# Performance work log

Measured on AMD Instinct MI355X. Metric: run time of the kernel, lower is better.

## Reference

```python
import jax, jax.numpy as jnp
import numpy as np

N_NODES = 100000
N_EDGES = 6400000
N_ELEMENTS = 95  # covalent radii table size
P = 6  # envelope polynomial order (init kwarg p)


def setup_inputs() -> dict:
    key = jax.random.key(0)
    k1, k2, k3, k4 = jax.random.split(key, 4)
    z = jax.random.randint(k1, (N_NODES,), 1, 95)  # atomic numbers 1..94
    edge_distance = jax.random.uniform(k2, (N_EDGES,), jnp.float32, 0.5, 5.0)
    edge_index = jax.random.randint(k3, (2, N_EDGES), 0, N_NODES)
    covalent_radii = jax.random.uniform(k4, (N_ELEMENTS,), jnp.float32, 0.5, 2.0)
    return {
        "z": z,
        "edge_distance": edge_distance,
        "edge_index": edge_index,
        "a_factor": jnp.float32(0.4546),
        "Z_power": jnp.float32(0.0842),
        "screen_coefs": jnp.full((4,), 0.1663, jnp.float32),
        "screen_exps": jnp.full((4,), 0.0354, jnp.float32),
        "covalent_radii": covalent_radii,
    }


def reference(z, edge_distance, edge_index, a_factor, Z_power, screen_coefs, screen_exps, covalent_radii):
    sender, receiver = edge_index[0], edge_index[1]
    Z_u = z[sender]
    Z_v = z[receiver]
    Z_uf = Z_u.astype(edge_distance.dtype)
    Z_vf = Z_v.astype(edge_distance.dtype)

    # screening length a = a_factor * 0.529 / (Zu^zp + Zv^zp)
    a = a_factor * 0.529 / (Z_uf ** Z_power + Z_vf ** Z_power)
    r_over_a = edge_distance / a  # [E]

    # phi(x) = sum_i c_i * exp(-d_i * x)
    phi = jnp.sum(screen_coefs * jnp.exp(-screen_exps * r_over_a[:, None]), axis=-1)  # [E]

    v_edges = 14.3996 * Z_uf * Z_vf / edge_distance * phi

    # smooth cutoff envelope
    r_max = covalent_radii[Z_u] + covalent_radii[Z_v]
    t = edge_distance / r_max
    p = float(P)
    envelope = (1.0
                - (p + 1.0) * (p + 2.0) / 2.0 * t ** P
                + p * (p + 2.0) * t ** (P + 1)
                - p * (p + 1.0) / 2.0 * t ** (P + 2))
    envelope = envelope * (t < 1.0).astype(edge_distance.dtype)

    v_edges = 0.5 * v_edges * envelope

    # scatter-add per receiver node
    V_ZBL = jax.ops.segment_sum(v_edges, receiver, num_segments=z.shape[0])
    return V_ZBL
```

## Files before the change

### kernel.cpp

```cpp
#include <hip/hip_runtime.h>

#define N_ELEM 95
#define MAX_NODES 100096
#define ZW_WORDS (MAX_NODES / 4)
#define RS2 20480
#define MAX_R2 5
#define EBLK 256

typedef float f32x4 __attribute__((ext_vector_type(4)));
typedef int   i32x4 __attribute__((ext_vector_type(4)));
typedef unsigned int u32;
typedef u32 u32x4 __attribute__((ext_vector_type(4)));
typedef unsigned short u16;

__device__ __forceinline__ u32 bf16_rtn(float f) {
    u32 u = __float_as_uint(f);
    return (u + 0x7FFFu + ((u >> 16) & 1u)) >> 16;
}
__device__ __forceinline__ u32 f15_rtn(float f) {
    u32 u = __float_as_uint(f);
    return (u + 0xFFFFu + ((u >> 17) & 1u)) >> 17;
}

__device__ __forceinline__ void build_ztab(
    u32* s_zw, const int* __restrict__ z, int n_words, int n_nodes, int tid, int nthr)
{
    for (int w = tid; w < n_words; w += nthr) {
        const int i = w << 2;
        u32 v;
        if (i + 4 <= n_nodes) {
            const i32x4 zz = ((const i32x4*)z)[w];
            v = ((u32)zz.x & 0xffu) | (((u32)zz.y & 0xffu) << 8)
              | (((u32)zz.z & 0xffu) << 16) | (((u32)zz.w & 0xffu) << 24);
        } else {
            v = 0u;
            for (int k = 0; k < 4 && i + k < n_nodes; ++k)
                v |= ((u32)z[i + k] & 0xffu) << (8 * k);
        }
        s_zw[w] = v;
    }
}

__global__ __launch_bounds__(1024) void k_edge_pack(
    const int*   __restrict__ z,
    const float* __restrict__ dist,
    const int*   __restrict__ sender,
    const int*   __restrict__ recv,
    const float* __restrict__ a_factor_p,
    const float* __restrict__ z_power_p,
    const float* __restrict__ coefs,
    const float* __restrict__ exps,
    const float* __restrict__ cradii,
    u32*         __restrict__ pk,
    int n_edges, int n_words, int n_nodes, int W)
{
    __shared__ u32    s_zw[ZW_WORDS];
    __shared__ float2 s_tab[N_ELEM];
    __shared__ float  s_coef[4], s_exp[4], s_inv;

    const int tid = threadIdx.x;
    build_ztab(s_zw, z, n_words, n_nodes, tid, 1024);
    if (tid < N_ELEM) {
        float zp = z_power_p[0];
        s_tab[tid] = make_float2(__powf((float)tid, zp), cradii[tid]);
    }
    if (tid < 4) { s_coef[tid] = coefs[tid]; s_exp[tid] = exps[tid]; }
    if (tid == 0) s_inv = 1.0f / (a_factor_p[0] * 0.529f);
    __syncthreads();

    const unsigned char* s_zb = (const unsigned char*)s_zw;
    const float inv_pref = s_inv;
    const float c0 = s_coef[0], c1 = s_coef[1], c2 = s_coef[2], c3 = s_coef[3];
    const float e0 = s_exp[0],  e1 = s_exp[1],  e2 = s_exp[2],  e3 = s_exp[3];

    const int n_grp = n_edges >> 3;
    const int g0 = blockIdx.x * W;
    const int g1 = min(n_grp, g0 + W);

    for (int g = g0 + tid; g < g1; g += 1024) {
        const f32x4 dA = __builtin_nontemporal_load((const f32x4*)dist + 2 * g);
        const f32x4 dB = __builtin_nontemporal_load((const f32x4*)dist + 2 * g + 1);
        const i32x4 sA = __builtin_nontemporal_load((const i32x4*)sender + 2 * g);
        const i32x4 sB = __builtin_nontemporal_load((const i32x4*)sender + 2 * g + 1);
        const i32x4 rA = __builtin_nontemporal_load((const i32x4*)recv + 2 * g);
        const i32x4 rB = __builtin_nontemporal_load((const i32x4*)recv + 2 * g + 1);

        float dd[8] = {dA.x, dA.y, dA.z, dA.w, dB.x, dB.y, dB.z, dB.w};
        int   ss[8] = {sA.x, sA.y, sA.z, sA.w, sB.x, sB.y, sB.z, sB.w};
        int   rr[8] = {rA.x, rA.y, rA.z, rA.w, rB.x, rB.y, rB.z, rB.w};

        int zu[8], zv[8];
        #pragma unroll
        for (int k = 0; k < 8; ++k) zu[k] = s_zb[ss[k]];
        #pragma unroll
        for (int k = 0; k < 8; ++k) zv[k] = s_zb[rr[k]];

        u32 ww[8];
        #pragma unroll
        for (int k = 0; k < 8; ++k) {
            const float d = dd[k];
            const float2 tu = s_tab[zu[k]];
            const float2 tv = s_tab[zv[k]];
            const float rmax = tu.y + tv.y;
            float o = 0.0f;
            if (d < rmax) {
                const float t   = __fdividef(d, rmax);
                const float roa = d * (tu.x + tv.x) * inv_pref;
                const float phi = c0 * __expf(-e0 * roa)
                                + c1 * __expf(-e1 * roa)
                                + c2 * __expf(-e2 * roa)
                                + c3 * __expf(-e3 * roa);
                const float v   = 7.1998f * (float)(zu[k] * zv[k]) * phi
                                * __fdividef(1.0f, d);
                const float t2  = t * t;
                const float t6  = t2 * t2 * t2;
                o = v * (1.0f - t6 * (28.0f - 48.0f * t + 21.0f * t2));
            }
            ww[k] = ((u32)rr[k] << 15) | f15_rtn(o);
        }
        ((u32x4*)pk)[2 * g]     = (u32x4){ww[0], ww[1], ww[2], ww[3]};
        ((u32x4*)pk)[2 * g + 1] = (u32x4){ww[4], ww[5], ww[6], ww[7]};
    }

    if (blockIdx.x == gridDim.x - 1) {
        for (int i = (n_grp << 3) + tid; i < n_edges; i += 1024) {
            const float d  = dist[i];
            const int   a  = s_zb[sender[i]];
            const u32   rv = (u32)recv[i];
            const int   b  = s_zb[rv];
            const float2 tu = s_tab[a];
            const float2 tv = s_tab[b];
            const float rmax = tu.y + tv.y;
            float o = 0.0f;
            if (d < rmax) {
                const float t   = __fdividef(d, rmax);
                const float roa = d * (tu.x + tv.x) * inv_pref;
                const float phi = c0 * __expf(-e0 * roa)
                                + c1 * __expf(-e1 * roa)
                                + c2 * __expf(-e2 * roa)
                                + c3 * __expf(-e3 * roa);
                const float v   = 7.1998f * (float)(a * b) * phi * __fdividef(1.0f, d);
                const float t2  = t * t;
                const float t6  = t2 * t2 * t2;
                o = v * (1.0f - t6 * (28.0f - 48.0f * t + 21.0f * t2));
            }
            pk[i] = (rv << 15) | f15_rtn(o);
        }
    }
}

__global__ __launch_bounds__(1024, 2) void k_accum4(
    const u32* __restrict__ pk,
    u16*       __restrict__ copies,
    int n_edges, int E8, int Q8, int C, int Rr)
{
    __shared__ float acc[RS2];
    const int c = blockIdx.x % C;
    const int r = blockIdx.x / C;
    const int tid = threadIdx.x;

    const u32 lo = (u32)r * RS2;
    const int q0 = c * Q8;
    const int q1 = min(E8, q0 + Q8);

    int q = q0 + tid;
    u32x4 wA = {0,0,0,0}, wB = {0,0,0,0};
    bool have = (q < q1);
    if (have) {
        wA = ((const u32x4*)pk)[2 * q];
        wB = ((const u32x4*)pk)[2 * q + 1];
    }

    for (int i = tid; i < RS2; i += 1024) acc[i] = 0.0f;
    __syncthreads();

    while (have) {
        const int qn = q + 1024;
        u32x4 nA = {0,0,0,0}, nB = {0,0,0,0};
        const bool hn = (qn < q1);
        if (hn) {
            nA = ((const u32x4*)pk)[2 * qn];
            nB = ((const u32x4*)pk)[2 * qn + 1];
        }
        u32 wv[8] = {wA.x, wA.y, wA.z, wA.w, wB.x, wB.y, wB.z, wB.w};
        #pragma unroll
        for (int k = 0; k < 8; ++k) {
            const u32 w   = wv[k];
            const u32 idx = (w >> 15) - lo;
            const u32 vb  = w & 0x7FFFu;
            if (idx < (u32)RS2 && vb)
                atomicAdd(&acc[idx], __uint_as_float(vb << 17));
        }
        wA = nA; wB = nB; q = qn; have = hn;
    }
    if (c == 0) {
        for (int e = (E8 << 3) + tid; e < n_edges; e += 1024) {
            const u32 w   = pk[e];
            const u32 idx = (w >> 15) - lo;
            const u32 vb  = w & 0x7FFFu;
            if (idx < (u32)RS2 && vb)
                atomicAdd(&acc[idx], __uint_as_float(vb << 17));
        }
    }
    __syncthreads();

    u16* __restrict__ dst = copies + ((size_t)c * Rr + r) * RS2;
    for (int i = tid * 8; i + 8 <= RS2; i += 8192) {
        const f32x4 a = *(const f32x4*)(acc + i);
        const f32x4 b = *(const f32x4*)(acc + i + 4);
        u32x4 o;
        o.x = bf16_rtn(a.x) | (bf16_rtn(a.y) << 16);
        o.y = bf16_rtn(a.z) | (bf16_rtn(a.w) << 16);
        o.z = bf16_rtn(b.x) | (bf16_rtn(b.y) << 16);
        o.w = bf16_rtn(b.z) | (bf16_rtn(b.w) << 16);
        *(u32x4*)(dst + i) = o;
    }
}

__global__ __launch_bounds__(256) void k_final4(
    const u32* __restrict__ copies32, float* __restrict__ out,
    int n_nodes, int C, int RRS32)
{
    const int p = blockIdx.x * 256 + threadIdx.x;
    const int n = p << 1;
    if (n < n_nodes) {
        float s0 = 0.0f, s1 = 0.0f;
        for (int c = 0; c < C; ++c) {
            const u32 w = copies32[(size_t)c * RRS32 + p];
            s0 += __uint_as_float(w << 16);
            s1 += __uint_as_float(w & 0xFFFF0000u);
        }
        if (n + 1 < n_nodes) {
            *(float2*)(out + n) = make_float2(s0, s1);
        } else {
            out[n] = s0;
        }
    }
}

__global__ __launch_bounds__(1024) void zbl_edge_lds(
    const int* __restrict__ z, const float* __restrict__ dist,
    const int* __restrict__ sender, const int* __restrict__ recv,
    const float* __restrict__ a_factor_p, const float* __restrict__ z_power_p,
    const float* __restrict__ coefs, const float* __restrict__ exps,
    const float* __restrict__ cradii, float* __restrict__ out,
    int n_edges, int n_words, int n_nodes)
{
    __shared__ u32    s_zw[ZW_WORDS];
    __shared__ float2 s_tab[N_ELEM];
    __shared__ float  s_coef[4], s_exp[4], s_inv;
    const int tid = threadIdx.x;
    build_ztab(s_zw, z, n_words, n_nodes, tid, 1024);
    if (tid < N_ELEM) {
        float zp = z_power_p[0];
        s_tab[tid] = make_float2(__powf((float)tid, zp), cradii[tid]);
    }
    if (tid < 4) { s_coef[tid] = coefs[tid]; s_exp[tid] = exps[tid]; }
    if (tid == 0) s_inv = 1.0f / (a_factor_p[0] * 0.529f);
    __syncthreads();
    const unsigned char* s_zb = (const unsigned char*)s_zw;
    const float inv_pref = s_inv;
    const int gstride = gridDim.x * 1024;
    for (int i = blockIdx.x * 1024 + tid; i < n_edges; i += gstride) {
        const float d  = dist[i];
        const int   a  = s_zb[sender[i]];
        const int   rv = recv[i];
        const int   b  = s_zb[rv];
        const float2 tu = s_tab[a];
        const float2 tv = s_tab[b];
        const float rmax = tu.y + tv.y;
        if (d < rmax) {
            const float t   = __fdividef(d, rmax);
            const float roa = d * (tu.x + tv.x) * inv_pref;
            const float phi = s_coef[0] * __expf(-s_exp[0] * roa)
                            + s_coef[1] * __expf(-s_exp[1] * roa)
                            + s_coef[2] * __expf(-s_exp[2] * roa)
                            + s_coef[3] * __expf(-s_exp[3] * roa);
            const float v   = 7.1998f * (float)(a * b) * phi * __fdividef(1.0f, d);
            const float t2  = t * t;
            const float t6  = t2 * t2 * t2;
            const float env = 1.0f - t6 * (28.0f - 48.0f * t + 21.0f * t2);
            unsafeAtomicAdd(&out[rv], v * env);
        }
    }
}

static inline size_t align16(size_t x) { return (x + 15) & ~(size_t)15; }

extern "C" void kernel_launch(void* const* d_in, const int* in_sizes, int n_in,
                              void* d_out, int out_size, void* d_ws, size_t ws_size,
                              hipStream_t stream) {
    const int*   z        = (const int*)d_in[0];
    const float* dist     = (const float*)d_in[1];
    const int*   eidx     = (const int*)d_in[2];
    const float* a_factor = (const float*)d_in[3];
    const float* z_power  = (const float*)d_in[4];
    const float* coefs    = (const float*)d_in[5];
    const float* exps     = (const float*)d_in[6];
    const float* cradii   = (const float*)d_in[7];
    float* out = (float*)d_out;

    const int n_edges = in_sizes[1];
    const int n_nodes = out_size;
    const int* sender = eidx;
    const int* recv   = eidx + n_edges;

    const int n_words = (n_nodes + 3) >> 2;
    const int R = (n_nodes + RS2 - 1) / RS2;

    const size_t off_pk  = 0;
    const size_t off_cop = align16((size_t)n_edges * sizeof(u32));

    int C = 0;
    if (R >= 1 && R <= MAX_R2 && n_nodes <= MAX_NODES) {
        C = 512 / R;
        while (C >= 4) {
            size_t need = off_cop + (size_t)C * R * RS2 * sizeof(u16);
            if (ws_size >= need) break;
            C = C * 3 / 4;
        }
        if (C < 4) C = 0;
    }

    if (C > 0) {
        char* ws = (char*)d_ws;
        u32* pkbuf  = (u32*)(ws + off_pk);
        u16* copies = (u16*)(ws + off_cop);

        const int n_grp = n_edges >> 3;
        const int W  = (n_grp + EBLK - 1) / EBLK;
        const int E8 = n_edges >> 3;
        const int Q8 = (E8 + C - 1) / C;

        k_edge_pack<<<EBLK, 1024, 0, stream>>>(
            z, dist, sender, recv, a_factor, z_power, coefs, exps, cradii,
            pkbuf, n_edges, n_words, n_nodes, W);
        k_accum4<<<C * R, 1024, 0, stream>>>(pkbuf, copies, n_edges, E8, Q8, C, R);
        k_final4<<<((n_nodes + 1) / 2 + 255) / 256, 256, 0, stream>>>(
            (const u32*)copies, out, n_nodes, C, (R * RS2) >> 1);
    } else if (n_nodes <= MAX_NODES) {
        hipMemsetAsync(out, 0, (size_t)n_nodes * sizeof(float), stream);
        zbl_edge_lds<<<256, 1024, 0, stream>>>(
            z, dist, sender, recv, a_factor, z_power, coefs, exps, cradii,
            out, n_edges, n_words, n_nodes);
    }
}
```

Baseline: 89.31 us.

## Bin cutoff-surviving edges by receiver range per block before LDS accumulation

The edge kernel now keeps only edges inside the cutoff radius. It uses a wavefront prefix scan and LDS counters to compact them into per-block, per-receiver-range segments of 16-bit local index plus bf16 value. It no longer writes a packed word for every edge. The accumulation kernel then reads only its own range's segments, instead of every range-block rescanning the whole packed edge array. The number of partial copies drops to a fixed 16, which shrinks the final reduction. Segments that overflow fall back to global atomics into a pre-zeroed output, so the output needs a memset and a read-modify-write in the final kernel. Values are also now rounded to bf16 where they were previously 15-bit floats.

```diff
diff --git a/kernel.cpp b/kernel.cpp
--- a/kernel.cpp
+++ b/kernel.cpp
@@ -6,20 +6,19 @@
 #define RS2 20480
 #define MAX_R2 5
 #define EBLK 256
+#define CAP 4096
+#define C_ACC 16
 
 typedef float f32x4 __attribute__((ext_vector_type(4)));
 typedef int   i32x4 __attribute__((ext_vector_type(4)));
 typedef unsigned int u32;
 typedef u32 u32x4 __attribute__((ext_vector_type(4)));
+typedef unsigned long long u64;
 typedef unsigned short u16;
 
 __device__ __forceinline__ u32 bf16_rtn(float f) {
     u32 u = __float_as_uint(f);
     return (u + 0x7FFFu + ((u >> 16) & 1u)) >> 16;
-}
-__device__ __forceinline__ u32 f15_rtn(float f) {
-    u32 u = __float_as_uint(f);
-    return (u + 0xFFFFu + ((u >> 17) & 1u)) >> 17;
 }
 
 __device__ __forceinline__ void build_ztab(
@@ -41,7 +40,7 @@
     }
 }
 
-__global__ __launch_bounds__(1024) void k_edge_pack(
+__global__ __launch_bounds__(1024) void k_edge_split(
     const int*   __restrict__ z,
     const float* __restrict__ dist,
     const int*   __restrict__ sender,
@@ -51,20 +50,28 @@
     const float* __restrict__ coefs,
     const float* __restrict__ exps,
     const float* __restrict__ cradii,
-    u32*         __restrict__ pk,
-    int n_edges, int n_words, int n_nodes, int W)
+    u32*         __restrict__ seg,
+    u32*         __restrict__ counts,
+    float*       __restrict__ out,
+    int n_edges, int n_words, int n_nodes, int W, int Rr)
 {
     __shared__ u32    s_zw[ZW_WORDS];
     __shared__ float2 s_tab[N_ELEM];
     __shared__ float  s_coef[4], s_exp[4], s_inv;
-
-    const int tid = threadIdx.x;
+    __shared__ u32    lcur[8];
+    __shared__ u32    s_base[16][8];
+
+    const int tid  = threadIdx.x;
+    const int lane = tid & 63;
+    const int wid  = tid >> 6;
+
     build_ztab(s_zw, z, n_words, n_nodes, tid, 1024);
     if (tid < N_ELEM) {
         float zp = z_power_p[0];
         s_tab[tid] = make_float2(__powf((float)tid, zp), cradii[tid]);
     }
     if (tid < 4) { s_coef[tid] = coefs[tid]; s_exp[tid] = exps[tid]; }
+    if (tid < 8) lcur[tid] = 0u;
     if (tid == 0) s_inv = 1.0f / (a_factor_p[0] * 0.529f);
     __syncthreads();
 
@@ -74,10 +81,15 @@
     const float e0 = s_exp[0],  e1 = s_exp[1],  e2 = s_exp[2],  e3 = s_exp[3];
 
     const int n_grp = n_edges >> 3;
-    const int g0 = blockIdx.x * W;
-    const int g1 = min(n_grp, g0 + W);
-
-    for (int g = g0 + tid; g < g1; g += 1024) {
+    const int b     = blockIdx.x;
+    const int g0    = b * W;
+    const int g1    = min(n_grp, g0 + W);
+
+    for (int gbase = g0; gbase < g1; gbase += 1024) {
+        const int  gg     = gbase + tid;
+        const bool active = (gg < g1);
+        const int  g      = active ? gg : (g1 - 1);
+
         const f32x4 dA = __builtin_nontemporal_load((const f32x4*)dist + 2 * g);
         const f32x4 dB = __builtin_nontemporal_load((const f32x4*)dist + 2 * g + 1);
         const i32x4 sA = __builtin_nontemporal_load((const i32x4*)sender + 2 * g);
@@ -95,15 +107,20 @@
         #pragma unroll
         for (int k = 0; k < 8; ++k) zv[k] = s_zb[rr[k]];
 
-        u32 ww[8];
+        bool  em[8];
+        float val[8];
+        u32   entry[8], rgk[8];
+        u64   cnt_pk = 0ull;
+
         #pragma unroll
         for (int k = 0; k < 8; ++k) {
             const float d = dd[k];
             const float2 tu = s_tab[zu[k]];
             const float2 tv = s_tab[zv[k]];
             const float rmax = tu.y + tv.y;
+            em[k] = active && (d < rmax);
             float o = 0.0f;
-            if (d < rmax) {
+            if (em[k]) {
                 const float t   = __fdividef(d, rmax);
                 const float roa = d * (tu.x + tv.x) * inv_pref;
                 const float phi = c0 * __expf(-e0 * roa)
@@ -116,22 +133,56 @@
                 const float t6  = t2 * t2 * t2;
                 o = v * (1.0f - t6 * (28.0f - 48.0f * t + 21.0f * t2));
             }
-            ww[k] = ((u32)rr[k] << 15) | f15_rtn(o);
-        }
-        ((u32x4*)pk)[2 * g]     = (u32x4){ww[0], ww[1], ww[2], ww[3]};
-        ((u32x4*)pk)[2 * g + 1] = (u32x4){ww[4], ww[5], ww[6], ww[7]};
-    }
-
-    if (blockIdx.x == gridDim.x - 1) {
+            val[k] = o;
+            const u32 rv  = (u32)rr[k];
+            const u32 rg  = rv / (u32)RS2;
+            rgk[k] = rg;
+            entry[k] = ((rv - rg * (u32)RS2) << 16) | bf16_rtn(o);
+            if (em[k]) cnt_pk += 1ull << (12 * rg);
+        }
+
+        u64 v = cnt_pk;
+        #pragma unroll
+        for (int d = 1; d < 64; d <<= 1) {
+            u64 t = __shfl_up(v, (unsigned)d, 64);
+            if (lane >= d) v += t;
+        }
+        const u64 excl = v - cnt_pk;
+
+        if (lane == 63) {
+            for (int r = 0; r < Rr; ++r) {
+                const u32 tot = (u32)(v >> (12 * r)) & 0xFFFu;
+                s_base[wid][r] = tot ? atomicAdd(&lcur[r], tot) : lcur[r];
+            }
+        }
+
+        u64 run_pk = 0ull;
+        #pragma unroll
+        for (int k = 0; k < 8; ++k) {
+            if (em[k]) {
+                const u32 rg  = rgk[k];
+                const u32 off = ((u32)(excl >> (12 * rg)) & 0xFFFu)
+                              + ((u32)(run_pk >> (12 * rg)) & 0xFFFu);
+                run_pk += 1ull << (12 * rg);
+                const u32 base = s_base[wid][rg];
+                const u32 pos  = base + off;
+                if (pos < (u32)CAP)
+                    seg[((size_t)b * Rr + rg) * CAP + pos] = entry[k];
+                else
+                    unsafeAtomicAdd(&out[rr[k]], val[k]);
+            }
+        }
+    }
+
+    if (b == gridDim.x - 1) {
         for (int i = (n_grp << 3) + tid; i < n_edges; i += 1024) {
             const float d  = dist[i];
             const int   a  = s_zb[sender[i]];
             const u32   rv = (u32)recv[i];
-            const int   b  = s_zb[rv];
+            const int   bb = s_zb[rv];
             const float2 tu = s_tab[a];
-            const float2 tv = s_tab[b];
+            const float2 tv = s_tab[bb];
             const float rmax = tu.y + tv.y;
-            float o = 0.0f;
             if (d < rmax) {
                 const float t   = __fdividef(d, rmax);
                 const float roa = d * (tu.x + tv.x) * inv_pref;
@@ -139,67 +190,46 @@
                                 + c1 * __expf(-e1 * roa)
                                 + c2 * __expf(-e2 * roa)
                                 + c3 * __expf(-e3 * roa);
-                const float v   = 7.1998f * (float)(a * b) * phi * __fdividef(1.0f, d);
+                const float v   = 7.1998f * (float)(a * bb) * phi * __fdividef(1.0f, d);
                 const float t2  = t * t;
                 const float t6  = t2 * t2 * t2;
-                o = v * (1.0f - t6 * (28.0f - 48.0f * t + 21.0f * t2));
+                const float o   = v * (1.0f - t6 * (28.0f - 48.0f * t + 21.0f * t2));
+                const u32 rg    = rv / (u32)RS2;
+                const u32 pos   = atomicAdd(&lcur[rg], 1u);
+                if (pos < (u32)CAP)
+                    seg[((size_t)b * Rr + rg) * CAP + pos] =
+                        ((rv - rg * (u32)RS2) << 16) | bf16_rtn(o);
+                else
+                    unsafeAtomicAdd(&out[rv], o);
             }
-            pk[i] = (rv << 15) | f15_rtn(o);
-        }
-    }
-}
-
-__global__ __launch_bounds__(1024, 2) void k_accum4(
-    const u32* __restrict__ pk,
+        }
+    }
+
+    __syncthreads();
+    if (tid < Rr)
+        counts[b * Rr + tid] = min(lcur[tid], (u32)CAP);
+}
+
+__global__ __launch_bounds__(1024) void k_gather_accum(
+    const u32* __restrict__ seg,
+    const u32* __restrict__ counts,
     u16*       __restrict__ copies,
-    int n_edges, int E8, int Q8, int C, int Rr)
+    int Rr)
 {
     __shared__ float acc[RS2];
-    const int c = blockIdx.x % C;
-    const int r = blockIdx.x / C;
+    const int c = blockIdx.x % C_ACC;
+    const int r = blockIdx.x / C_ACC;
     const int tid = threadIdx.x;
 
-    const u32 lo = (u32)r * RS2;
-    const int q0 = c * Q8;
-    const int q1 = min(E8, q0 + Q8);
-
-    int q = q0 + tid;
-    u32x4 wA = {0,0,0,0}, wB = {0,0,0,0};
-    bool have = (q < q1);
-    if (have) {
-        wA = ((const u32x4*)pk)[2 * q];
-        wB = ((const u32x4*)pk)[2 * q + 1];
-    }
-
     for (int i = tid; i < RS2; i += 1024) acc[i] = 0.0f;
     __syncthreads();
 
-    while (have) {
-        const int qn = q + 1024;
-        u32x4 nA = {0,0,0,0}, nB = {0,0,0,0};
-        const bool hn = (qn < q1);
-        if (hn) {
-            nA = ((const u32x4*)pk)[2 * qn];
-            nB = ((const u32x4*)pk)[2 * qn + 1];
-        }
-        u32 wv[8] = {wA.x, wA.y, wA.z, wA.w, wB.x, wB.y, wB.z, wB.w};
-        #pragma unroll
-        for (int k = 0; k < 8; ++k) {
-            const u32 w   = wv[k];
-            const u32 idx = (w >> 15) - lo;
-            const u32 vb  = w & 0x7FFFu;
-            if (idx < (u32)RS2 && vb)
-                atomicAdd(&acc[idx], __uint_as_float(vb << 17));
-        }
-        wA = nA; wB = nB; q = qn; have = hn;
-    }
-    if (c == 0) {
-        for (int e = (E8 << 3) + tid; e < n_edges; e += 1024) {
-            const u32 w   = pk[e];
-            const u32 idx = (w >> 15) - lo;
-            const u32 vb  = w & 0x7FFFu;
-            if (idx < (u32)RS2 && vb)
-                atomicAdd(&acc[idx], __uint_as_float(vb << 17));
+    for (int b = c; b < EBLK; b += C_ACC) {
+        const u32 cnt = counts[b * Rr + r];
+        const u32* __restrict__ p = seg + ((size_t)b * Rr + r) * CAP;
+        for (u32 i = tid; i < cnt; i += 1024) {
+            const u32 w = p[i];
+            atomicAdd(&acc[w >> 16], __uint_as_float((w & 0xFFFFu) << 16));
         }
     }
     __syncthreads();
@@ -217,7 +247,7 @@
     }
 }
 
-__global__ __launch_bounds__(256) void k_final4(
+__global__ __launch_bounds__(256) void k_final5(
     const u32* __restrict__ copies32, float* __restrict__ out,
     int n_nodes, int C, int RRS32)
 {
@@ -225,15 +255,17 @@
     const int n = p << 1;
     if (n < n_nodes) {
         float s0 = 0.0f, s1 = 0.0f;
+        #pragma unroll 4
         for (int c = 0; c < C; ++c) {
             const u32 w = copies32[(size_t)c * RRS32 + p];
             s0 += __uint_as_float(w << 16);
             s1 += __uint_as_float(w & 0xFFFF0000u);
         }
         if (n + 1 < n_nodes) {
-            *(float2*)(out + n) = make_float2(s0, s1);
+            const float2 prev = *(const float2*)(out + n);
+            *(float2*)(out + n) = make_float2(prev.x + s0, prev.y + s1);
         } else {
-            out[n] = s0;
+            out[n] += s0;
         }
     }
 }
@@ -308,38 +340,29 @@
     const int n_words = (n_nodes + 3) >> 2;
     const int R = (n_nodes + RS2 - 1) / RS2;
 
-    const size_t off_pk  = 0;
-    const size_t off_cop = align16((size_t)n_edges * sizeof(u32));
-
-    int C = 0;
-    if (R >= 1 && R <= MAX_R2 && n_nodes <= MAX_NODES) {
-        C = 512 / R;
-        while (C >= 4) {
-            size_t need = off_cop + (size_t)C * R * RS2 * sizeof(u16);
-            if (ws_size >= need) break;
-            C = C * 3 / 4;
-        }
-        if (C < 4) C = 0;
-    }
-
-    if (C > 0) {
+    const size_t seg_bytes = (size_t)EBLK * R * CAP * sizeof(u32);
+    const size_t off_cnt   = align16(seg_bytes);
+    const size_t off_cop   = align16(off_cnt + (size_t)EBLK * R * sizeof(u32));
+    const size_t need      = off_cop + (size_t)C_ACC * R * RS2 * sizeof(u16);
+
+    hipMemsetAsync(out, 0, (size_t)n_nodes * sizeof(float), stream);
+
+    if (R >= 1 && R <= MAX_R2 && n_nodes <= MAX_NODES && ws_size >= need) {
         char* ws = (char*)d_ws;
-        u32* pkbuf  = (u32*)(ws + off_pk);
+        u32* seg    = (u32*)ws;
+        u32* counts = (u32*)(ws + off_cnt);
         u16* copies = (u16*)(ws + off_cop);
 
         const int n_grp = n_edges >> 3;
-        const int W  = (n_grp + EBLK - 1) / EBLK;
-        const int E8 = n_edges >> 3;
-        const int Q8 = (E8 + C - 1) / C;
-
-        k_edge_pack<<<EBLK, 1024, 0, stream>>>(
+        const int W = (n_grp + EBLK - 1) / EBLK;
+
+        k_edge_split<<<EBLK, 1024, 0, stream>>>(
             z, dist, sender, recv, a_factor, z_power, coefs, exps, cradii,
-            pkbuf, n_edges, n_words, n_nodes, W);
-        k_accum4<<<C * R, 1024, 0, stream>>>(pkbuf, copies, n_edges, E8, Q8, C, R);
-        k_final4<<<((n_nodes + 1) / 2 + 255) / 256, 256, 0, stream>>>(
-            (const u32*)copies, out, n_nodes, C, (R * RS2) >> 1);
+            seg, counts, out, n_edges, n_words, n_nodes, W, R);
+        k_gather_accum<<<C_ACC * R, 1024, 0, stream>>>(seg, counts, copies, R);
+        k_final5<<<((n_nodes + 1) / 2 + 255) / 256, 256, 0, stream>>>(
+            (const u32*)copies, out, n_nodes, C_ACC, (R * RS2) >> 1);
     } else if (n_nodes <= MAX_NODES) {
-        hipMemsetAsync(out, 0, (size_t)n_nodes * sizeof(float), stream);
         zbl_edge_lds<<<256, 1024, 0, stream>>>(
             z, dist, sender, recv, a_factor, z_power, coefs, exps, cradii,
             out, n_edges, n_words, n_nodes);
```

Result: slower. 97.70 us (+9.4%).
